# Kernel tuning notes

Hardware: AMD Instinct MI355X
Metric: run time of the kernel (lower is better)

## Reference

```python
import jax, jax.numpy as jnp
import numpy as np

N = 50000
E = 800000
IN = 256
HID = 64
HEADS = 4
EPS = 1e-5


def batchnorm(x, g, b):
    # training-mode BatchNorm1d over node dim, biased variance (torch semantics)
    mu = jnp.mean(x, axis=0)
    var = jnp.mean((x - mu) ** 2, axis=0)
    return (x - mu) * jax.lax.rsqrt(var + EPS) * g + b


def gat(x, edge_index, W, a_src, a_dst, bias, heads, out_ch, num_nodes):
    src, dst = edge_index[0], edge_index[1]
    h = (x @ W).reshape(num_nodes, heads, out_ch)          # [N,H,C]
    al_s = jnp.einsum('nhc,hc->nh', h, a_src)              # [N,H]
    al_d = jnp.einsum('nhc,hc->nh', h, a_dst)
    e = jax.nn.leaky_relu(al_s[src] + al_d[dst], 0.2)      # [E,H]
    # segment softmax over destination neighborhoods
    m = jax.ops.segment_max(e, dst, num_segments=num_nodes)
    m = jnp.where(jnp.isfinite(m), m, 0.0)
    ex = jnp.exp(e - m[dst])                               # [E,H]
    denom = jax.ops.segment_sum(ex, dst, num_segments=num_nodes)
    alpha = ex / (denom[dst] + 1e-16)                      # [E,H]
    msg = alpha[:, :, None] * h[src]                       # [E,H,C]
    out = jax.ops.segment_sum(msg, dst, num_segments=num_nodes)
    return out.reshape(num_nodes, heads * out_ch) + bias


def setup_inputs() -> dict:
    key = jax.random.key(0)
    ks = jax.random.split(key, 12)
    d = {}
    d['x'] = jax.random.normal(ks[0], (N, IN), jnp.float32)
    d['edge_index'] = jax.random.randint(ks[1], (2, E), 0, N, jnp.int32)
    d['bn1_g'] = jnp.ones((IN,), jnp.float32)
    d['bn1_b'] = jnp.zeros((IN,), jnp.float32)
    d['lin1_W'] = jax.random.normal(ks[2], (IN, HID * HEADS), jnp.float32) * (1.0 / np.sqrt(IN))
    d['lin1_b'] = jnp.zeros((HID * HEADS,), jnp.float32)
    d['con1_W'] = jax.random.normal(ks[3], (IN, HID * HEADS), jnp.float32) * (1.0 / np.sqrt(IN))
    d['con1_asrc'] = jax.random.normal(ks[4], (HEADS, HID), jnp.float32) * 0.1
    d['con1_adst'] = jax.random.normal(ks[5], (HEADS, HID), jnp.float32) * 0.1
    d['con1_b'] = jnp.zeros((HID * HEADS,), jnp.float32)
    d['bn3_g'] = jnp.ones((HID * HEADS,), jnp.float32)
    d['bn3_b'] = jnp.zeros((HID * HEADS,), jnp.float32)
    d['lin3_W'] = jax.random.normal(ks[6], (HID * HEADS, 2), jnp.float32) * (1.0 / np.sqrt(HID * HEADS))
    d['lin3_b'] = jnp.zeros((2,), jnp.float32)
    d['con3_W'] = jax.random.normal(ks[7], (HID * HEADS, 2), jnp.float32) * (1.0 / np.sqrt(HID * HEADS))
    d['con3_asrc'] = jax.random.normal(ks[8], (1, 2), jnp.float32) * 0.1
    d['con3_adst'] = jax.random.normal(ks[9], (1, 2), jnp.float32) * 0.1
    d['con3_b'] = jnp.zeros((2,), jnp.float32)
    return d


def reference(x, edge_index, bn1_g, bn1_b, lin1_W, lin1_b, con1_W, con1_asrc, con1_adst, con1_b,
              bn3_g, bn3_b, lin3_W, lin3_b, con3_W, con3_asrc, con3_adst, con3_b):
    x = batchnorm(x, bn1_g, bn1_b)
    x = jax.nn.relu(x @ lin1_W + lin1_b
                    + gat(x, edge_index, con1_W, con1_asrc, con1_adst, con1_b, HEADS, HID, N))
    x = batchnorm(x, bn3_g, bn3_b)
    x = jax.nn.relu(x @ lin3_W + lin3_b
                    + gat(x, edge_index, con3_W, con3_asrc, con3_adst, con3_b, 1, 2, N))
    return x
```

## Files before the change

### kernel.cpp

```cpp
#include <hip/hip_runtime.h>
#include <math.h>

#define NN 50000
#define NE 800000
#define IC 256
#define EPS 1e-5f

typedef __attribute__((ext_vector_type(8))) short short8;
typedef __attribute__((ext_vector_type(4))) float f32x4;

enum : int {
  OFF_S1     = 0,
  OFF_S2     = 256,
  OFF_COUNTS = 512,
  ZERO_END   = OFF_COUNTS + 50000,
  OFF_CURSOR = ZERO_END,
  OFF_START  = OFF_CURSOR + 50000,
  OFF_BSUM   = OFF_START + 50004,
  OFF_BOFF   = OFF_BSUM + 64,
  OFF_ALS    = OFF_BOFF + 64,
  OFF_ALD    = OFF_ALS + 200000,
  OFF_SRCS   = OFF_ALD + 200000,
  OFF_Y32    = OFF_SRCS + 800000,
  OFF_ND4    = OFF_Y32 + 100000,
  OFF_BFH    = OFF_ND4 + 200000,
  OFF_BFL    = OFF_BFH + 65536,
  OFF_HBF    = OFF_BFL + 65536,
  OFF_YLBF   = OFF_HBF + 6400000,
  WS_FLOATS  = OFF_YLBF + 6400000
};

__device__ __forceinline__ float lrelu(float s) { return s > 0.f ? s : 0.2f * s; }
__device__ __forceinline__ float b2f(unsigned short u) {
  return __uint_as_float(((unsigned)u) << 16);
}
__device__ __forceinline__ unsigned short f2bf(float f) {
  unsigned u = __float_as_uint(f);
  return (unsigned short)((u + 0x7fffu + ((u >> 16) & 1u)) >> 16);
}

__global__ __launch_bounds__(256) void k_bnstats(const float* __restrict__ x,
                                                 float* __restrict__ S1,
                                                 float* __restrict__ S2) {
  int c = threadIdx.x;
  float s1 = 0.f, s2 = 0.f;
  for (int r = blockIdx.x; r < NN; r += gridDim.x) {
    float v = x[r * IC + c];
    s1 += v;
    s2 = fmaf(v, v, s2);
  }
  atomicAdd(&S1[c], s1);
  atomicAdd(&S2[c], s2);
}

__global__ __launch_bounds__(256) void k_bnstats2(const unsigned short* __restrict__ x1,
                                                  float* __restrict__ S1,
                                                  float* __restrict__ S2) {
  int c = threadIdx.x;
  float s1 = 0.f, s2 = 0.f;
  for (int r = blockIdx.x; r < NN; r += gridDim.x) {
    float v = b2f(x1[r * IC + c]);
    s1 += v;
    s2 = fmaf(v, v, s2);
  }
  atomicAdd(&S1[c], s1);
  atomicAdd(&S2[c], s2);
}

__global__ __launch_bounds__(256) void k_prepB(const float* __restrict__ Wlin,
                                               const float* __restrict__ Wcon,
                                               unsigned short* __restrict__ Bfh,
                                               unsigned short* __restrict__ Bfl) {
  int id = blockIdx.x * 256 + threadIdx.x;
  int j = id & 7, lane = (id >> 3) & 63, nt = (id >> 9) & 31, ks = id >> 14;
  int k = ks * 32 + ((lane >> 4) << 3) + j;
  int n = nt * 16 + (lane & 15);
  float v = (n < 256) ? Wlin[k * 256 + n] : Wcon[k * 256 + (n - 256)];
  unsigned short h = f2bf(v);
  Bfh[id] = h;
  Bfl[id] = f2bf(v - b2f(h));
}

__global__ __launch_bounds__(256, 2) void k_gemm(const float* __restrict__ x,
                                                 const float* __restrict__ S1,
                                                 const float* __restrict__ S2,
                                                 const float* __restrict__ bng,
                                                 const float* __restrict__ bnb,
                                                 const unsigned short* __restrict__ Bfh,
                                                 const unsigned short* __restrict__ Bfl,
                                                 unsigned short* __restrict__ ylbf,
                                                 unsigned short* __restrict__ hbf,
                                                 const float* __restrict__ asrc,
                                                 const float* __restrict__ adst,
                                                 float* __restrict__ als,
                                                 float* __restrict__ ald) {
  __shared__ unsigned short Ah[2048], Al[2048];
  __shared__ float sc[256], sh[256];
  const int tid = threadIdx.x;
  const int row0 = blockIdx.x * 64;
  const int wave = tid >> 6, lane = tid & 63;
  {
    float mu = S1[tid] * (1.f / NN);
    float var = S2[tid] * (1.f / NN) - mu * mu;
    float ss = bng[tid] / sqrtf(var + EPS);
    sc[tid] = ss;
    sh[tid] = bnb[tid] - mu * ss;
  }
  const float4* x4 = (const float4*)x;
  const short8* Bh8 = (const short8*)Bfh;
  const short8* Bl8 = (const short8*)Bfl;
  f32x4 acc[4][8];
#pragma unroll
  for (int i = 0; i < 4; ++i)
#pragma unroll
    for (int j = 0; j < 8; ++j) acc[i][j] = (f32x4){0.f, 0.f, 0.f, 0.f};

  const int m = tid >> 2, kg = tid & 3;
  const int r = row0 + m;
  const int aaddr = (((m >> 4) * 64) + ((m & 15) | (kg << 4))) * 8;
  __syncthreads();

  for (int ks = 0; ks < 8; ++ks) {
    const int c0 = ks * 32 + kg * 8;
    float v[8];
    if (r < NN) {
      int base = (r * IC + c0) >> 2;
      float4 fa = x4[base], fb = x4[base + 1];
      v[0] = fa.x; v[1] = fa.y; v[2] = fa.z; v[3] = fa.w;
      v[4] = fb.x; v[5] = fb.y; v[6] = fb.z; v[7] = fb.w;
#pragma unroll
      for (int j = 0; j < 8; ++j) v[j] = fmaf(v[j], sc[c0 + j], sh[c0 + j]);
    } else {
#pragma unroll
      for (int j = 0; j < 8; ++j) v[j] = 0.f;
    }
    unsigned ph[4], pl[4];
#pragma unroll
    for (int j = 0; j < 4; ++j) {
      unsigned short h0 = f2bf(v[2 * j]), h1 = f2bf(v[2 * j + 1]);
      unsigned short l0 = f2bf(v[2 * j] - b2f(h0));
      unsigned short l1 = f2bf(v[2 * j + 1] - b2f(h1));
      ph[j] = (unsigned)h0 | ((unsigned)h1 << 16);
      pl[j] = (unsigned)l0 | ((unsigned)l1 << 16);
    }
    *(uint4*)&Ah[aaddr] = make_uint4(ph[0], ph[1], ph[2], ph[3]);
    *(uint4*)&Al[aaddr] = make_uint4(pl[0], pl[1], pl[2], pl[3]);
    __syncthreads();

    short8 ah[4], alo[4];
#pragma unroll
    for (int mt = 0; mt < 4; ++mt) {
      ah[mt] = *(const short8*)&Ah[(mt * 64 + lane) * 8];
      alo[mt] = *(const short8*)&Al[(mt * 64 + lane) * 8];
    }
#pragma unroll
    for (int nt = 0; nt < 8; ++nt) {
      int boff = (ks * 32 + wave * 8 + nt) * 64 + lane;
      short8 bh = Bh8[boff];
      short8 bl = Bl8[boff];
#pragma unroll
      for (int mt = 0; mt < 4; ++mt) {
        acc[mt][nt] = __builtin_amdgcn_mfma_f32_16x16x32_bf16(ah[mt], bh, acc[mt][nt], 0, 0, 0);
        acc[mt][nt] = __builtin_amdgcn_mfma_f32_16x16x32_bf16(alo[mt], bh, acc[mt][nt], 0, 0, 0);
        acc[mt][nt] = __builtin_amdgcn_mfma_f32_16x16x32_bf16(ah[mt], bl, acc[mt][nt], 0, 0, 0);
      }
    }
    __syncthreads();
  }
  const int colq = lane & 15, quad = lane >> 4;
  if (wave < 2) {
#pragma unroll
    for (int mt = 0; mt < 4; ++mt)
#pragma unroll
      for (int reg = 0; reg < 4; ++reg) {
        int rr = row0 + mt * 16 + quad * 4 + reg;
        if (rr < NN) {
#pragma unroll
          for (int nt = 0; nt < 8; ++nt)
            ylbf[rr * IC + wave * 128 + nt * 16 + colq] = f2bf(acc[mt][nt][reg]);
        }
      }
  } else {
    const int wh = wave - 2;
    const int headA = wh * 2, headB = wh * 2 + 1;
    float asA[4], asB[4], adA[4], adB[4];
#pragma unroll
    for (int j = 0; j < 4; ++j) {
      asA[j] = asrc[headA * 64 + j * 16 + colq];
      asB[j] = asrc[headB * 64 + j * 16 + colq];
      adA[j] = adst[headA * 64 + j * 16 + colq];
      adB[j] = adst[headB * 64 + j * 16 + colq];
    }
#pragma unroll
    for (int mt = 0; mt < 4; ++mt)
#pragma unroll
      for (int reg = 0; reg < 4; ++reg) {
        int rr = row0 + mt * 16 + quad * 4 + reg;
        float sA = 0.f, sB = 0.f, dA = 0.f, dB = 0.f;
#pragma unroll
        for (int j = 0; j < 4; ++j) {
          float hA = acc[mt][j][reg], hB = acc[mt][j + 4][reg];
          sA = fmaf(hA, asA[j], sA);
          sB = fmaf(hB, asB[j], sB);
          dA = fmaf(hA, adA[j], dA);
          dB = fmaf(hB, adB[j], dB);
          if (rr < NN) {
            hbf[rr * IC + wh * 128 + j * 16 + colq] = f2bf(hA);
            hbf[rr * IC + wh * 128 + (j + 4) * 16 + colq] = f2bf(hB);
          }
        }
#pragma unroll
        for (int off = 1; off < 16; off <<= 1) {
          sA += __shfl_xor(sA, off, 64);
          sB += __shfl_xor(sB, off, 64);
          dA += __shfl_xor(dA, off, 64);
          dB += __shfl_xor(dB, off, 64);
        }
        if (rr < NN) {
          if (colq == 0) als[rr * 4 + headA] = sA;
          else if (colq == 1) als[rr * 4 + headB] = sB;
          else if (colq == 2) ald[rr * 4 + headA] = dA;
          else if (colq == 3) ald[rr * 4 + headB] = dB;
        }
      }
  }
}

__global__ __launch_bounds__(256) void k_hist(const int* __restrict__ dst,
                                              int* __restrict__ counts) {
  int e = blockIdx.x * 256 + threadIdx.x;
  atomicAdd(&counts[dst[e]], 1);
}

__global__ __launch_bounds__(1024) void k_scanA(const int* __restrict__ counts,
                                                int* __restrict__ start,
                                                int* __restrict__ bsum) {
  __shared__ int buf[1024];
  int b = blockIdx.x, tid = threadIdx.x;
  int i = b * 1024 + tid;
  int v = (i < NN) ? counts[i] : 0;
  buf[tid] = v;
  __syncthreads();
  for (int off = 1; off < 1024; off <<= 1) {
    int t = (tid >= off) ? buf[tid - off] : 0;
    __syncthreads();
    buf[tid] += t;
    __syncthreads();
  }
  if (i < NN) start[i] = buf[tid] - v;
  if (tid == 1023) bsum[b] = buf[1023];
}

__global__ __launch_bounds__(64) void k_scanB(const int* __restrict__ bsum,
                                              int* __restrict__ boff,
                                              int* __restrict__ start,
                                              float* __restrict__ S1,
                                              float* __restrict__ S2) {
  int l = threadIdx.x;
  for (int i = l; i < 256; i += 64) {
    S1[i] = 0.f;
    S2[i] = 0.f;
  }
  int v = (l < 49) ? bsum[l] : 0;
  int incl = v;
#pragma unroll
  for (int off = 1; off < 64; off <<= 1) {
    int t = __shfl_up(incl, off, 64);
    if (l >= off) incl += t;
  }
  if (l < 49) boff[l] = incl - v;
  if (l == 48) start[NN] = incl;
}

__global__ __launch_bounds__(1024) void k_scanC(int* __restrict__ start,
                                                int* __restrict__ cursor,
                                                const int* __restrict__ boff) {
  int i = blockIdx.x * 1024 + threadIdx.x;
  if (i < NN) {
    int s = start[i] + boff[blockIdx.x];
    start[i] = s;
    cursor[i] = s;
  }
}

__global__ __launch_bounds__(256) void k_scatter(const int* __restrict__ src,
                                                 const int* __restrict__ dst,
                                                 int* __restrict__ cursor,
                                                 int* __restrict__ srcs) {
  int e = blockIdx.x * 256 + threadIdx.x;
  int pos = atomicAdd(&cursor[dst[e]], 1);
  srcs[pos] = src[e];
}

__global__ __launch_bounds__(256) void k_agg(const ushort4* __restrict__ hq,
                                             ushort4* __restrict__ x1,
                                             const float4* __restrict__ als4,
                                             const float4* __restrict__ ald4,
                                             const int* __restrict__ start,
                                             const int* __restrict__ srcs,
                                             const float4* __restrict__ lb4,
                                             const float4* __restrict__ cb4) {
  __shared__ float lsp[1024];
  const int tid = threadIdx.x;
  const int wave = tid >> 6, lane = tid & 63, head = lane >> 4;
  const int n = blockIdx.x * 4 + wave;
  const float* als = (const float*)als4;
  const int s = start[n], t = start[n + 1];
  const int deg = t - s;
  const float4 aldv = ald4[n];
  int svk = -1;
  float e0 = -INFINITY, e1 = -INFINITY, e2 = -INFINITY, e3 = -INFINITY;
  if (lane < deg) {
    svk = srcs[s + lane];
    float4 a = als4[svk];
    e0 = lrelu(a.x + aldv.x);
    e1 = lrelu(a.y + aldv.y);
    e2 = lrelu(a.z + aldv.z);
    e3 = lrelu(a.w + aldv.w);
  }
  float m0 = e0, m1 = e1, m2 = e2, m3 = e3;
  if (deg > 64) {
    for (int i = s + 64 + lane; i < t; i += 64) {
      float4 a = als4[srcs[i]];
      m0 = fmaxf(m0, lrelu(a.x + aldv.x));
      m1 = fmaxf(m1, lrelu(a.y + aldv.y));
      m2 = fmaxf(m2, lrelu(a.z + aldv.z));
      m3 = fmaxf(m3, lrelu(a.w + aldv.w));
    }
  }
#pragma unroll
  for (int off = 1; off < 64; off <<= 1) {
    m0 = fmaxf(m0, __shfl_xor(m0, off, 64));
    m1 = fmaxf(m1, __shfl_xor(m1, off, 64));
    m2 = fmaxf(m2, __shfl_xor(m2, off, 64));
    m3 = fmaxf(m3, __shfl_xor(m3, off, 64));
  }
  float p0 = 0.f, p1 = 0.f, p2 = 0.f, p3 = 0.f;
  if (svk >= 0) {
    p0 = __expf(e0 - m0);
    p1 = __expf(e1 - m1);
    p2 = __expf(e2 - m2);
    p3 = __expf(e3 - m3);
  }
  *(float4*)&lsp[wave * 256 + lane * 4] = make_float4(p0, p1, p2, p3);
  float d0 = p0, d1 = p1, d2 = p2, d3 = p3;
  const float aldh = head == 0 ? aldv.x : head == 1 ? aldv.y : head == 2 ? aldv.z : aldv.w;
  const float mh = head == 0 ? m0 : head == 1 ? m1 : head == 2 ? m2 : m3;
  if (deg > 64) {
    for (int i = s + 64 + lane; i < t; i += 64) {
      float4 a = als4[srcs[i]];
      d0 += __expf(lrelu(a.x + aldv.x) - m0);
      d1 += __expf(lrelu(a.y + aldv.y) - m1);
      d2 += __expf(lrelu(a.z + aldv.z) - m2);
      d3 += __expf(lrelu(a.w + aldv.w) - m3);
    }
  }
#pragma unroll
  for (int off = 1; off < 64; off <<= 1) {
    d0 += __shfl_xor(d0, off, 64);
    d1 += __shfl_xor(d1, off, 64);
    d2 += __shfl_xor(d2, off, 64);
    d3 += __shfl_xor(d3, off, 64);
  }
  const float inv =
      1.f / ((head == 0 ? d0 : head == 1 ? d1 : head == 2 ? d2 : d3) + 1e-16f);
  float a0 = 0.f, a1 = 0.f, a2 = 0.f, a3 = 0.f;
  const int cnt = min(deg, 64);
  const int wbase = wave * 256 + head;
  int j = 0;
  for (; j + 4 <= cnt; j += 4) {
    int sv0 = __shfl(svk, j, 64), sv1 = __shfl(svk, j + 1, 64);
    int sv2 = __shfl(svk, j + 2, 64), sv3 = __shfl(svk, j + 3, 64);
    ushort4 hv0 = hq[sv0 * 64 + lane];
    ushort4 hv1 = hq[sv1 * 64 + lane];
    ushort4 hv2 = hq[sv2 * 64 + lane];
    ushort4 hv3 = hq[sv3 * 64 + lane];
    float w0 = lsp[wbase + j * 4], w1 = lsp[wbase + j * 4 + 4];
    float w2 = lsp[wbase + j * 4 + 8], w3 = lsp[wbase + j * 4 + 12];
    a0 = fmaf(w0, b2f(hv0.x), a0); a1 = fmaf(w0, b2f(hv0.y), a1);
    a2 = fmaf(w0, b2f(hv0.z), a2); a3 = fmaf(w0, b2f(hv0.w), a3);
    a0 = fmaf(w1, b2f(hv1.x), a0); a1 = fmaf(w1, b2f(hv1.y), a1);
    a2 = fmaf(w1, b2f(hv1.z), a2); a3 = fmaf(w1, b2f(hv1.w), a3);
    a0 = fmaf(w2, b2f(hv2.x), a0); a1 = fmaf(w2, b2f(hv2.y), a1);
    a2 = fmaf(w2, b2f(hv2.z), a2); a3 = fmaf(w2, b2f(hv2.w), a3);
    a0 = fmaf(w3, b2f(hv3.x), a0); a1 = fmaf(w3, b2f(hv3.y), a1);
    a2 = fmaf(w3, b2f(hv3.z), a2); a3 = fmaf(w3, b2f(hv3.w), a3);
  }
  for (; j < cnt; ++j) {
    int sv = __shfl(svk, j, 64);
    float w = lsp[wbase + j * 4];
    ushort4 hv = hq[sv * 64 + lane];
    a0 = fmaf(w, b2f(hv.x), a0);
    a1 = fmaf(w, b2f(hv.y), a1);
    a2 = fmaf(w, b2f(hv.z), a2);
    a3 = fmaf(w, b2f(hv.w), a3);
  }
  if (deg > 64) {
    for (int i = s + 64; i < t; ++i) {
      int sv = srcs[i];
      float av = als[sv * 4 + head];
      float p = __expf(lrelu(av + aldh) - mh);
      ushort4 hv = hq[sv * 64 + lane];
      a0 = fmaf(p, b2f(hv.x), a0);
      a1 = fmaf(p, b2f(hv.y), a1);
      a2 = fmaf(p, b2f(hv.z), a2);
      a3 = fmaf(p, b2f(hv.w), a3);
    }
  }
  ushort4 yb = x1[n * 64 + lane];
  float4 bb1 = lb4[lane], bb2 = cb4[lane];
  ushort4 rb;
  rb.x = f2bf(fmaxf(fmaf(a0, inv, b2f(yb.x) + bb1.x + bb2.x), 0.f));
  rb.y = f2bf(fmaxf(fmaf(a1, inv, b2f(yb.y) + bb1.y + bb2.y), 0.f));
  rb.z = f2bf(fmaxf(fmaf(a2, inv, b2f(yb.z) + bb1.z + bb2.z), 0.f));
  rb.w = f2bf(fmaxf(fmaf(a3, inv, b2f(yb.w) + bb1.w + bb2.w), 0.f));
  x1[n * 64 + lane] = rb;
}

__global__ __launch_bounds__(256) void k_node2(const ushort4* __restrict__ x1,
                                               const float* __restrict__ S1,
                                               const float* __restrict__ S2,
                                               const float* __restrict__ g3,
                                               const float* __restrict__ b3,
                                               const float4* __restrict__ Wl4,
                                               const float4* __restrict__ Wc4,
                                               const float* __restrict__ a3s,
                                               const float* __restrict__ a3d,
                                               const float* __restrict__ l3b,
                                               const float* __restrict__ c3b,
                                               float2* __restrict__ y32,
                                               float4* __restrict__ nd4) {
  __shared__ float sc[256], sh[256];
  const int tid = threadIdx.x;
  {
    float mu = S1[tid] * (1.f / NN);
    float var = S2[tid] * (1.f / NN) - mu * mu;
    float ss = g3[tid] / sqrtf(var + EPS);
    sc[tid] = ss;
    sh[tid] = b3[tid] - mu * ss;
  }
  __syncthreads();
  const int n = blockIdx.x * 4 + (tid >> 6);
  const int lane = tid & 63;
  ushort4 xb = x1[n * 64 + lane];
  float x0 = fmaf(b2f(xb.x), sc[lane * 4 + 0], sh[lane * 4 + 0]);
  float x1v = fmaf(b2f(xb.y), sc[lane * 4 + 1], sh[lane * 4 + 1]);
  float x2 = fmaf(b2f(xb.z), sc[lane * 4 + 2], sh[lane * 4 + 2]);
  float x3 = fmaf(b2f(xb.w), sc[lane * 4 + 3], sh[lane * 4 + 3]);
  float4 wa = Wl4[lane * 2], wb = Wl4[lane * 2 + 1];
  float y0 = x0 * wa.x + x1v * wa.z + x2 * wb.x + x3 * wb.z;
  float y1 = x0 * wa.y + x1v * wa.w + x2 * wb.y + x3 * wb.w;
  float4 ca = Wc4[lane * 2], cb = Wc4[lane * 2 + 1];
  float g0 = x0 * ca.x + x1v * ca.z + x2 * cb.x + x3 * cb.z;
  float g1 = x0 * ca.y + x1v * ca.w + x2 * cb.y + x3 * cb.w;
#pragma unroll
  for (int off = 1; off < 64; off <<= 1) {
    y0 += __shfl_xor(y0, off, 64);
    y1 += __shfl_xor(y1, off, 64);
    g0 += __shfl_xor(g0, off, 64);
    g1 += __shfl_xor(g1, off, 64);
  }
  if (lane == 0) {
    y32[n] = make_float2(y0 + l3b[0] + c3b[0], y1 + l3b[1] + c3b[1]);
    nd4[n] = make_float4(g0 * a3s[0] + g1 * a3s[1], g0, g1,
                         g0 * a3d[0] + g1 * a3d[1]);
  }
}

__global__ __launch_bounds__(256) void k_final(const int* __restrict__ start,
                                               const int* __restrict__ srcs,
                                               const float4* __restrict__ nd4,
                                               const float2* __restrict__ y32,
                                               float* __restrict__ out) {
  const int tid = threadIdx.x;
  const int n = blockIdx.x * 16 + (tid >> 4);
  const int li = tid & 15;
  const int s = start[n], t = start[n + 1];
  const float ad = nd4[n].w;
  float4 v[4];
  bool val[4];
#pragma unroll
  for (int kk = 0; kk < 4; ++kk) {
    int ii = s + li + kk * 16;
    val[kk] = ii < t;
    v[kk] = val[kk] ? nd4[srcs[ii]] : make_float4(0.f, 0.f, 0.f, 0.f);
  }
  float m = -INFINITY;
#pragma unroll
  for (int kk = 0; kk < 4; ++kk)
    if (val[kk]) m = fmaxf(m, lrelu(v[kk].x + ad));
  if (t - s > 64)
    for (int ii = s + 64 + li; ii < t; ii += 16)
      m = fmaxf(m, lrelu(nd4[srcs[ii]].x + ad));
#pragma unroll
  for (int off = 1; off < 16; off <<= 1) m = fmaxf(m, __shfl_xor(m, off, 64));
  float den = 0.f, a0 = 0.f, a1 = 0.f;
#pragma unroll
  for (int kk = 0; kk < 4; ++kk)
    if (val[kk]) {
      float p = __expf(lrelu(v[kk].x + ad) - m);
      den += p;
      a0 = fmaf(p, v[kk].y, a0);
      a1 = fmaf(p, v[kk].z, a1);
    }
  if (t - s > 64)
    for (int ii = s + 64 + li; ii < t; ii += 16) {
      float4 vv = nd4[srcs[ii]];
      float p = __expf(lrelu(vv.x + ad) - m);
      den += p;
      a0 = fmaf(p, vv.y, a0);
      a1 = fmaf(p, vv.z, a1);
    }
#pragma unroll
  for (int off = 1; off < 16; off <<= 1) {
    den += __shfl_xor(den, off, 64);
    a0 += __shfl_xor(a0, off, 64);
    a1 += __shfl_xor(a1, off, 64);
  }
  if (li == 0) {
    float2 y = y32[n];
    float inv = 1.f / (den + 1e-16f);
    out[2 * n] = fmaxf(fmaf(a0, inv, y.x), 0.f);
    out[2 * n + 1] = fmaxf(fmaf(a1, inv, y.y), 0.f);
  }
}

extern "C" void kernel_launch(void* const* d_in, const int* in_sizes, int n_in,
                              void* d_out, int out_size, void* d_ws, size_t ws_size,
                              hipStream_t stream) {
  const float* x = (const float*)d_in[0];
  const int* ei = (const int*)d_in[1];
  const float* bn1_g = (const float*)d_in[2];
  const float* bn1_b = (const float*)d_in[3];
  const float* lin1_W = (const float*)d_in[4];
  const float* lin1_b = (const float*)d_in[5];
  const float* con1_W = (const float*)d_in[6];
  const float* con1_as = (const float*)d_in[7];
  const float* con1_ad = (const float*)d_in[8];
  const float* con1_b = (const float*)d_in[9];
  const float* bn3_g = (const float*)d_in[10];
  const float* bn3_b = (const float*)d_in[11];
  const float* lin3_W = (const float*)d_in[12];
  const float* lin3_b = (const float*)d_in[13];
  const float* con3_W = (const float*)d_in[14];
  const float* con3_as = (const float*)d_in[15];
  const float* con3_ad = (const float*)d_in[16];
  const float* con3_b = (const float*)d_in[17];
  float* ws = (float*)d_ws;
  const int* srcA = ei;
  const int* dstA = ei + NE;

  float* S1 = ws + OFF_S1;
  float* S2 = ws + OFF_S2;
  int* counts = (int*)(ws + OFF_COUNTS);
  int* cursor = (int*)(ws + OFF_CURSOR);
  int* start = (int*)(ws + OFF_START);
  int* bsum = (int*)(ws + OFF_BSUM);
  int* boff = (int*)(ws + OFF_BOFF);
  float* als = ws + OFF_ALS;
  float* ald = ws + OFF_ALD;
  int* srcs = (int*)(ws + OFF_SRCS);
  float2* y32 = (float2*)(ws + OFF_Y32);
  float4* nd4 = (float4*)(ws + OFF_ND4);
  unsigned short* Bfh = (unsigned short*)(ws + OFF_BFH);
  unsigned short* Bfl = (unsigned short*)(ws + OFF_BFL);
  unsigned short* hbf = (unsigned short*)(ws + OFF_HBF);
  unsigned short* ylbf = (unsigned short*)(ws + OFF_YLBF);

  hipMemsetAsync(ws, 0, (size_t)ZERO_END * sizeof(float), stream);

  k_prepB<<<512, 256, 0, stream>>>(lin1_W, con1_W, Bfh, Bfl);
  k_bnstats<<<1024, 256, 0, stream>>>(x, S1, S2);
  k_gemm<<<782, 256, 0, stream>>>(x, S1, S2, bn1_g, bn1_b, Bfh, Bfl, ylbf, hbf,
                                  con1_as, con1_ad, als, ald);
  k_hist<<<3125, 256, 0, stream>>>(dstA, counts);
  k_scanA<<<49, 1024, 0, stream>>>(counts, start, bsum);
  k_scanB<<<1, 64, 0, stream>>>(bsum, boff, start, S1, S2);
  k_scanC<<<49, 1024, 0, stream>>>(start, cursor, boff);
  k_scatter<<<3125, 256, 0, stream>>>(srcA, dstA, cursor, srcs);
  k_agg<<<12500, 256, 0, stream>>>((const ushort4*)hbf, (ushort4*)ylbf,
                                   (const float4*)als, (const float4*)ald, start,
                                   srcs, (const float4*)lin1_b,
                                   (const float4*)con1_b);
  k_bnstats2<<<1024, 256, 0, stream>>>(ylbf, S1, S2);
  k_node2<<<12500, 256, 0, stream>>>((const ushort4*)ylbf, S1, S2, bn3_g, bn3_b,
                                     (const float4*)lin3_W, (const float4*)con3_W,
                                     con3_as, con3_ad, lin3_b, con3_b, y32, nd4);
  k_final<<<3125, 256, 0, stream>>>(start, srcs, nd4, y32, (float*)d_out);
}
```

Baseline: 450.7 us.

## Split GEMM output columns across blocks, fuse stats with histogram, merge scans

The GEMM is split into two column halves per row tile (grid 2x782), which halves accumulator registers per thread and allows four blocks per CU. The cost is that each half reloads and re-converts the same A tile. BatchNorm statistics and the destination histogram now run as one launch, and the single-block bsum scan is folded into scanC so each block computes its own offset. The last two changes remove kernel launches and per-launch serialization, in exchange for redundant A-side work in the GEMM.

```diff
diff --git a/kernel.cpp b/kernel.cpp
--- a/kernel.cpp
+++ b/kernel.cpp
@@ -39,18 +39,26 @@
   return (unsigned short)((u + 0x7fffu + ((u >> 16) & 1u)) >> 16);
 }
 
-__global__ __launch_bounds__(256) void k_bnstats(const float* __restrict__ x,
-                                                 float* __restrict__ S1,
-                                                 float* __restrict__ S2) {
-  int c = threadIdx.x;
-  float s1 = 0.f, s2 = 0.f;
-  for (int r = blockIdx.x; r < NN; r += gridDim.x) {
-    float v = x[r * IC + c];
-    s1 += v;
-    s2 = fmaf(v, v, s2);
-  }
-  atomicAdd(&S1[c], s1);
-  atomicAdd(&S2[c], s2);
+__global__ __launch_bounds__(256) void k_statshist(const float* __restrict__ x,
+                                                   float* __restrict__ S1,
+                                                   float* __restrict__ S2,
+                                                   const int* __restrict__ dst,
+                                                   int* __restrict__ counts) {
+  int b = blockIdx.x;
+  if (b < 1024) {
+    int c = threadIdx.x;
+    float s1 = 0.f, s2 = 0.f;
+    for (int r = b; r < NN; r += 1024) {
+      float v = x[r * IC + c];
+      s1 += v;
+      s2 = fmaf(v, v, s2);
+    }
+    atomicAdd(&S1[c], s1);
+    atomicAdd(&S2[c], s2);
+  } else {
+    int e = (b - 1024) * 256 + threadIdx.x;
+    atomicAdd(&counts[dst[e]], 1);
+  }
 }
 
 __global__ __launch_bounds__(256) void k_bnstats2(const unsigned short* __restrict__ x1,
@@ -81,7 +89,7 @@
   Bfl[id] = f2bf(v - b2f(h));
 }
 
-__global__ __launch_bounds__(256, 2) void k_gemm(const float* __restrict__ x,
+__global__ __launch_bounds__(256, 4) void k_gemm(const float* __restrict__ x,
                                                  const float* __restrict__ S1,
                                                  const float* __restrict__ S2,
                                                  const float* __restrict__ bng,
@@ -97,7 +105,8 @@
   __shared__ unsigned short Ah[2048], Al[2048];
   __shared__ float sc[256], sh[256];
   const int tid = threadIdx.x;
-  const int row0 = blockIdx.x * 64;
+  const int bn = blockIdx.x;
+  const int row0 = blockIdx.y * 64;
   const int wave = tid >> 6, lane = tid & 63;
   {
     float mu = S1[tid] * (1.f / NN);
@@ -109,11 +118,11 @@
   const float4* x4 = (const float4*)x;
   const short8* Bh8 = (const short8*)Bfh;
   const short8* Bl8 = (const short8*)Bfl;
-  f32x4 acc[4][8];
+  f32x4 acc[4][4];
 #pragma unroll
   for (int i = 0; i < 4; ++i)
 #pragma unroll
-    for (int j = 0; j < 8; ++j) acc[i][j] = (f32x4){0.f, 0.f, 0.f, 0.f};
+    for (int j = 0; j < 4; ++j) acc[i][j] = (f32x4){0.f, 0.f, 0.f, 0.f};
 
   const int m = tid >> 2, kg = tid & 3;
   const int r = row0 + m;
@@ -154,8 +163,8 @@
       alo[mt] = *(const short8*)&Al[(mt * 64 + lane) * 8];
     }
 #pragma unroll
-    for (int nt = 0; nt < 8; ++nt) {
-      int boff = (ks * 32 + wave * 8 + nt) * 64 + lane;
+    for (int nt = 0; nt < 4; ++nt) {
+      int boff = (ks * 32 + bn * 16 + wave * 4 + nt) * 64 + lane;
       short8 bh = Bh8[boff];
       short8 bl = Bl8[boff];
 #pragma unroll
@@ -168,7 +177,7 @@
     __syncthreads();
   }
   const int colq = lane & 15, quad = lane >> 4;
-  if (wave < 2) {
+  if (bn == 0) {
 #pragma unroll
     for (int mt = 0; mt < 4; ++mt)
 #pragma unroll
@@ -176,60 +185,42 @@
         int rr = row0 + mt * 16 + quad * 4 + reg;
         if (rr < NN) {
 #pragma unroll
-          for (int nt = 0; nt < 8; ++nt)
-            ylbf[rr * IC + wave * 128 + nt * 16 + colq] = f2bf(acc[mt][nt][reg]);
+          for (int nt = 0; nt < 4; ++nt)
+            ylbf[rr * IC + wave * 64 + nt * 16 + colq] = f2bf(acc[mt][nt][reg]);
         }
       }
   } else {
-    const int wh = wave - 2;
-    const int headA = wh * 2, headB = wh * 2 + 1;
-    float asA[4], asB[4], adA[4], adB[4];
+    const int head = wave;
+    float asv[4], adv[4];
 #pragma unroll
     for (int j = 0; j < 4; ++j) {
-      asA[j] = asrc[headA * 64 + j * 16 + colq];
-      asB[j] = asrc[headB * 64 + j * 16 + colq];
-      adA[j] = adst[headA * 64 + j * 16 + colq];
-      adB[j] = adst[headB * 64 + j * 16 + colq];
+      asv[j] = asrc[head * 64 + j * 16 + colq];
+      adv[j] = adst[head * 64 + j * 16 + colq];
     }
 #pragma unroll
     for (int mt = 0; mt < 4; ++mt)
 #pragma unroll
       for (int reg = 0; reg < 4; ++reg) {
         int rr = row0 + mt * 16 + quad * 4 + reg;
-        float sA = 0.f, sB = 0.f, dA = 0.f, dB = 0.f;
+        float sA = 0.f, dA = 0.f;
 #pragma unroll
         for (int j = 0; j < 4; ++j) {
-          float hA = acc[mt][j][reg], hB = acc[mt][j + 4][reg];
-          sA = fmaf(hA, asA[j], sA);
-          sB = fmaf(hB, asB[j], sB);
-          dA = fmaf(hA, adA[j], dA);
-          dB = fmaf(hB, adB[j], dB);
-          if (rr < NN) {
-            hbf[rr * IC + wh * 128 + j * 16 + colq] = f2bf(hA);
-            hbf[rr * IC + wh * 128 + (j + 4) * 16 + colq] = f2bf(hB);
-          }
+          float hA = acc[mt][j][reg];
+          sA = fmaf(hA, asv[j], sA);
+          dA = fmaf(hA, adv[j], dA);
+          if (rr < NN) hbf[rr * IC + head * 64 + j * 16 + colq] = f2bf(hA);
         }
 #pragma unroll
         for (int off = 1; off < 16; off <<= 1) {
           sA += __shfl_xor(sA, off, 64);
-          sB += __shfl_xor(sB, off, 64);
           dA += __shfl_xor(dA, off, 64);
-          dB += __shfl_xor(dB, off, 64);
         }
         if (rr < NN) {
-          if (colq == 0) als[rr * 4 + headA] = sA;
-          else if (colq == 1) als[rr * 4 + headB] = sB;
-          else if (colq == 2) ald[rr * 4 + headA] = dA;
-          else if (colq == 3) ald[rr * 4 + headB] = dB;
+          if (colq == 0) als[rr * 4 + head] = sA;
+          else if (colq == 1) ald[rr * 4 + head] = dA;
         }
       }
   }
-}
-
-__global__ __launch_bounds__(256) void k_hist(const int* __restrict__ dst,
-                                              int* __restrict__ counts) {
-  int e = blockIdx.x * 256 + threadIdx.x;
-  atomicAdd(&counts[dst[e]], 1);
 }
 
 __global__ __launch_bounds__(1024) void k_scanA(const int* __restrict__ counts,
@@ -251,33 +242,32 @@
   if (tid == 1023) bsum[b] = buf[1023];
 }
 
-__global__ __launch_bounds__(64) void k_scanB(const int* __restrict__ bsum,
-                                              int* __restrict__ boff,
-                                              int* __restrict__ start,
-                                              float* __restrict__ S1,
-                                              float* __restrict__ S2) {
-  int l = threadIdx.x;
-  for (int i = l; i < 256; i += 64) {
-    S1[i] = 0.f;
-    S2[i] = 0.f;
-  }
-  int v = (l < 49) ? bsum[l] : 0;
-  int incl = v;
-#pragma unroll
-  for (int off = 1; off < 64; off <<= 1) {
-    int t = __shfl_up(incl, off, 64);
-    if (l >= off) incl += t;
-  }
-  if (l < 49) boff[l] = incl - v;
-  if (l == 48) start[NN] = incl;
-}
-
 __global__ __launch_bounds__(1024) void k_scanC(int* __restrict__ start,
                                                 int* __restrict__ cursor,
-                                                const int* __restrict__ boff) {
-  int i = blockIdx.x * 1024 + threadIdx.x;
+                                                const int* __restrict__ bsum,
+                                                float* __restrict__ S1,
+                                                float* __restrict__ S2) {
+  __shared__ int sboff;
+  int tid = threadIdx.x;
+  if (tid < 64) {
+    int v = (tid < 49) ? bsum[tid] : 0;
+    int incl = v;
+#pragma unroll
+    for (int off = 1; off < 64; off <<= 1) {
+      int t = __shfl_up(incl, off, 64);
+      if (tid >= off) incl += t;
+    }
+    if (tid == blockIdx.x) sboff = incl - v;
+    if (blockIdx.x == 0 && tid == 48) start[NN] = incl;
+  }
+  if (blockIdx.x == 0 && tid < 256) {
+    S1[tid] = 0.f;
+    S2[tid] = 0.f;
+  }
+  __syncthreads();
+  int i = blockIdx.x * 1024 + tid;
   if (i < NN) {
-    int s = start[i] + boff[blockIdx.x];
+    int s = start[i] + sboff;
     start[i] = s;
     cursor[i] = s;
   }
@@ -556,7 +546,6 @@
   int* cursor = (int*)(ws + OFF_CURSOR);
   int* start = (int*)(ws + OFF_START);
   int* bsum = (int*)(ws + OFF_BSUM);
-  int* boff = (int*)(ws + OFF_BOFF);
   float* als = ws + OFF_ALS;
   float* ald = ws + OFF_ALD;
   int* srcs = (int*)(ws + OFF_SRCS);
@@ -570,13 +559,11 @@
   hipMemsetAsync(ws, 0, (size_t)ZERO_END * sizeof(float), stream);
 
   k_prepB<<<512, 256, 0, stream>>>(lin1_W, con1_W, Bfh, Bfl);
-  k_bnstats<<<1024, 256, 0, stream>>>(x, S1, S2);
-  k_gemm<<<782, 256, 0, stream>>>(x, S1, S2, bn1_g, bn1_b, Bfh, Bfl, ylbf, hbf,
-                                  con1_as, con1_ad, als, ald);
-  k_hist<<<3125, 256, 0, stream>>>(dstA, counts);
+  k_statshist<<<1024 + 3125, 256, 0, stream>>>(x, S1, S2, dstA, counts);
+  k_gemm<<<dim3(2, 782), 256, 0, stream>>>(x, S1, S2, bn1_g, bn1_b, Bfh, Bfl, ylbf,
+                                           hbf, con1_as, con1_ad, als, ald);
   k_scanA<<<49, 1024, 0, stream>>>(counts, start, bsum);
-  k_scanB<<<1, 64, 0, stream>>>(bsum, boff, start, S1, S2);
-  k_scanC<<<49, 1024, 0, stream>>>(start, cursor, boff);
+  k_scanC<<<49, 1024, 0, stream>>>(start, cursor, bsum, S1, S2);
   k_scatter<<<3125, 256, 0, stream>>>(srcA, dstA, cursor, srcs);
   k_agg<<<12500, 256, 0, stream>>>((const ushort4*)hbf, (ushort4*)ylbf,
                                    (const float4*)als, (const float4*)ald, start,
```

After: 435.1 us. 1.04x faster.
